# Kernel optimization log

Hardware: AMD Instinct MI355X
Metric: run time of the kernel (lower is better)

The kernel has to match this reference:

```python
import jax, jax.numpy as jnp
import numpy as np

N_NODES = 50000
N_EDGES = 150000
D = 512
N_LAYERS = 4
BN_EPS = 1e-5


def setup_inputs() -> dict:
    key = jax.random.key(0)
    ks = jax.random.split(key, 8)
    scale = 1.0 / np.sqrt(D)
    x = jax.random.normal(ks[0], (N_NODES, D), dtype=jnp.float32)
    W1 = jax.random.normal(ks[1], (N_LAYERS, D, D), dtype=jnp.float32) * scale
    b1 = jax.random.normal(ks[2], (N_LAYERS, D), dtype=jnp.float32) * 0.01
    gamma = jnp.ones((N_LAYERS, D), dtype=jnp.float32)
    beta = jnp.zeros((N_LAYERS, D), dtype=jnp.float32)
    W2 = jax.random.normal(ks[3], (N_LAYERS, D, D), dtype=jnp.float32) * scale
    b2 = jax.random.normal(ks[4], (N_LAYERS, D), dtype=jnp.float32) * 0.01
    src = jax.random.randint(ks[5], (N_EDGES,), 0, N_NODES, dtype=jnp.int32)
    dst = jax.random.randint(ks[6], (N_EDGES,), 0, N_NODES, dtype=jnp.int32)
    return {"x": x, "W1": W1, "b1": b1, "gamma": gamma, "beta": beta,
            "W2": W2, "b2": b2, "src": src, "dst": dst}


def _gin_layer(h, src, dst, W1, b1, gamma, beta, W2, b2):
    # GIN sum aggregation: agg[v] = sum_{(u->v) in E} h[u]; eps = 0
    agg = jax.ops.segment_sum(h[src], dst, num_segments=N_NODES)
    z = jnp.dot(h + agg, W1.T) + b1                      # [N, D] Linear1
    # BatchNorm1d (training mode: batch stats, biased variance)
    mu = jnp.mean(z, axis=0)
    var = jnp.mean(jnp.square(z - mu), axis=0)
    z = (z - mu) * jax.lax.rsqrt(var + BN_EPS) * gamma + beta
    z = jax.nn.relu(z)
    return jnp.dot(z, W2.T) + b2                          # [N, D] Linear2


def reference(x, W1, b1, gamma, beta, W2, b2, src, dst):
    h = x
    outs = []
    for i in range(N_LAYERS):
        h = _gin_layer(h, src, dst, W1[i], b1[i], gamma[i], beta[i], W2[i], b2[i])
        outs.append(h)
    # single graph: dgl.mean_nodes == mean over all nodes, squeeze -> [D]
    return (jnp.mean(outs[-1], axis=0), jnp.mean(outs[-2], axis=0))
```

## Files before the change

### kernel.cpp

```cpp
#include <hip/hip_runtime.h>

#define NN 50000
#define MPAD 50176
#define DD 512
#define NE 150000

typedef float f32x2 __attribute__((ext_vector_type(2)));
typedef float f32x4 __attribute__((ext_vector_type(4)));
typedef float f32x8 __attribute__((ext_vector_type(8)));
typedef __bf16 bf16x8 __attribute__((ext_vector_type(8)));
typedef unsigned short u16x8 __attribute__((ext_vector_type(8)));
typedef unsigned int u32x2 __attribute__((ext_vector_type(2)));

__device__ __forceinline__ void gload16(const void* g, void* l) {
  __builtin_amdgcn_global_load_lds((const __attribute__((address_space(1))) void*)g,
                                   (__attribute__((address_space(3))) void*)l, 16, 0, 0);
}

__device__ __forceinline__ u32x2 f32x8_to_fp8(f32x8 v) {
  int t0 = __builtin_amdgcn_cvt_pk_fp8_f32(v[0], v[1], 0, false);
  t0 = __builtin_amdgcn_cvt_pk_fp8_f32(v[2], v[3], t0, true);
  int t1 = __builtin_amdgcn_cvt_pk_fp8_f32(v[4], v[5], 0, false);
  t1 = __builtin_amdgcn_cvt_pk_fp8_f32(v[6], v[7], t1, true);
  u32x2 r;
  r[0] = (unsigned)t0;
  r[1] = (unsigned)t1;
  return r;
}
__device__ __forceinline__ f32x8 fp8x8_to_f32(u32x2 u) {
  f32x2 a = __builtin_amdgcn_cvt_pk_f32_fp8((int)u[0], false);
  f32x2 b = __builtin_amdgcn_cvt_pk_f32_fp8((int)u[0], true);
  f32x2 c = __builtin_amdgcn_cvt_pk_f32_fp8((int)u[1], false);
  f32x2 d = __builtin_amdgcn_cvt_pk_f32_fp8((int)u[1], true);
  f32x8 v;
  v[0]=a[0]; v[1]=a[1]; v[2]=b[0]; v[3]=b[1]; v[4]=c[0]; v[5]=c[1]; v[6]=d[0]; v[7]=d[1];
  return v;
}

#define READ_FRAGS(la, lb, kk, AV, BV)                                                       \
  {                                                                                          \
    const int so = (((kk) * 4 + fg) ^ sx) * 8;                                               \
    _Pragma("unroll") for (int i = 0; i < 4; ++i)                                            \
        AV[i] = *reinterpret_cast<const bf16x8*>(&(la)[(rg + i * 16 + fr) * 64 + so]);       \
    _Pragma("unroll") for (int j = 0; j < 4; ++j)                                            \
        BV[j] = *reinterpret_cast<const bf16x8*>(&(lb)[(cg + j * 16 + fr) * 64 + so]);       \
  }

#define MFMA16(AV, BV)                                                                       \
  _Pragma("unroll") for (int i = 0; i < 4; ++i)                                              \
      _Pragma("unroll") for (int j = 0; j < 4; ++j)                                          \
          acc[i][j] = __builtin_amdgcn_mfma_f32_16x16x32_bf16(AV[i], BV[j], acc[i][j], 0, 0, 0);

#define PHASE_TAIL(AV, BV)                                                                   \
  __builtin_amdgcn_s_barrier();                                                              \
  asm volatile("s_waitcnt lgkmcnt(0)" ::: "memory");                                         \
  __builtin_amdgcn_sched_barrier(0);                                                         \
  __builtin_amdgcn_s_setprio(1);                                                             \
  MFMA16(AV, BV);                                                                            \
  __builtin_amdgcn_s_setprio(0);

__global__ __launch_bounds__(256) void prep1_k(
    const float* __restrict__ x, const float* __restrict__ W1,
    const int* __restrict__ dst, unsigned char* __restrict__ xq,
    unsigned short* __restrict__ wb1, int* __restrict__ cnt,
    unsigned short* __restrict__ xact, float* __restrict__ stats,
    float* __restrict__ cs2, float* __restrict__ cs3) {
  const int b = blockIdx.x;
  const int tid = threadIdx.x;
  if (b < 12500) {
    const size_t i = ((size_t)b * 256 + tid) * 8;
    const f32x4* g = reinterpret_cast<const f32x4*>(x + i);
    f32x4 a = g[0], c = g[1];
    f32x8 v;
    v[0]=a[0]; v[1]=a[1]; v[2]=a[2]; v[3]=a[3]; v[4]=c[0]; v[5]=c[1]; v[6]=c[2]; v[7]=c[3];
    *reinterpret_cast<u32x2*>(xq + i) = f32x8_to_fp8(v);
  } else if (b < 12628) {
    const size_t i = ((size_t)(b - 12500) * 256 + tid) * 8;
    const f32x4* g = reinterpret_cast<const f32x4*>(W1 + i);
    f32x4 a = g[0], c = g[1];
    f32x8 v;
    v[0]=a[0]; v[1]=a[1]; v[2]=a[2]; v[3]=a[3]; v[4]=c[0]; v[5]=c[1]; v[6]=c[2]; v[7]=c[3];
    *reinterpret_cast<bf16x8*>(wb1 + i) = __builtin_convertvector(v, bf16x8);
  } else if (b < 13214) {
    const int e = (b - 12628) * 256 + tid;
    if (e < NE) atomicAdd(&cnt[dst[e]], 1);
  } else if (b < 13258) {
    const int i = (b - 13214) * 256 + tid;
    u16x8 zz = {};
    *reinterpret_cast<u16x8*>(xact + (size_t)NN * DD + (size_t)i * 8) = zz;
  } else {
    for (int i = tid; i < 2 * DD; i += 256) stats[i] = 0.f;
    for (int i = tid; i < DD; i += 256) {
      cs2[i] = 0.f;
      cs3[i] = 0.f;
    }
  }
}

__global__ __launch_bounds__(1024) void scan_k(const int* __restrict__ cnt,
                                               int* __restrict__ rowptr,
                                               int* __restrict__ cursor) {
  __shared__ int wsum[16];
  __shared__ int base_s;
  if (threadIdx.x == 0) base_s = 0;
  __syncthreads();
  const int lane = threadIdx.x & 63;
  const int wid = threadIdx.x >> 6;
  for (int c0 = 0; c0 < NN; c0 += 1024) {
    const int i = c0 + threadIdx.x;
    const int v = (i < NN) ? cnt[i] : 0;
    int incl = v;
#pragma unroll
    for (int d = 1; d < 64; d <<= 1) {
      int t = __shfl_up(incl, d);
      if (lane >= d) incl += t;
    }
    if (lane == 63) wsum[wid] = incl;
    __syncthreads();
    if (wid == 0 && lane < 16) {
      int wv = wsum[lane];
#pragma unroll
      for (int d = 1; d < 16; d <<= 1) {
        int t = __shfl_up(wv, d);
        if (lane >= d) wv += t;
      }
      wsum[lane] = wv;
    }
    __syncthreads();
    const int waveoff = wid ? wsum[wid - 1] : 0;
    const int excl = base_s + waveoff + incl - v;
    if (i < NN) {
      rowptr[i] = excl;
      cursor[i] = excl;
    }
    __syncthreads();
    if (threadIdx.x == 0) base_s += wsum[15];
    __syncthreads();
  }
  if (threadIdx.x == 0) rowptr[NN] = base_s;
}

__global__ __launch_bounds__(256) void prep2_k(
    const int* __restrict__ src, const int* __restrict__ dst,
    int* __restrict__ cursor, int* __restrict__ csrc,
    const float* __restrict__ W2, float* __restrict__ W2T) {
  __shared__ float t[64][65];
  const int b = blockIdx.x;
  const int tid = threadIdx.x;
  if (b < 586) {
    const int e = b * 256 + tid;
    if (e < NE) {
      const int pos = atomicAdd(&cursor[dst[e]], 1);
      csrc[pos] = src[e];
    }
  } else {
    const int q = b - 586;
    const int l = q >> 6;
    const int rem = q & 63;
    const int a0 = (rem >> 3) * 64;
    const int b0 = (rem & 7) * 64;
    const float* sp = W2 + (size_t)l * DD * DD;
    float* dp = W2T + (size_t)l * DD * DD;
#pragma unroll
    for (int k = 0; k < 16; ++k) {
      const int idx = k * 256 + tid;
      const int r = idx >> 6, c = idx & 63;
      t[r][c] = sp[(size_t)(a0 + r) * DD + b0 + c];
    }
    __syncthreads();
#pragma unroll
    for (int k = 0; k < 16; ++k) {
      const int idx = k * 256 + tid;
      const int r = idx >> 6, c = idx & 63;
      dp[(size_t)(b0 + r) * DD + a0 + c] = t[c][r];
    }
  }
}

__global__ __launch_bounds__(256) void prep3_k(
    const float* __restrict__ W1all, const float* __restrict__ W2T,
    unsigned short* __restrict__ WF, const float* __restrict__ b2all,
    float* __restrict__ cvec, const int* __restrict__ rowptr,
    float* __restrict__ degp1) {
  __shared__ char pl[36864];
  const int b = blockIdx.x;
  const int tid = threadIdx.x;
  if (b < 48) {
    constexpr int LDK = 72;
    unsigned short* lA = (unsigned short*)pl;
    unsigned short* lB = (unsigned short*)(pl + 18432);
    const int l = b >> 4;
    const int rem = b & 15;
    const int brow = (rem >> 2) * 128;
    const int bcol = (rem & 3) * 128;
    const float* A = W1all + (size_t)(l + 1) * DD * DD;
    const float* Bt = W2T + (size_t)l * DD * DD;
    unsigned short* out = WF + (size_t)l * DD * DD;
    const int lane = tid & 63;
    const int w = tid >> 6;
    const int wr = (w >> 1) * 64;
    const int wc = (w & 1) * 64;
    const int fr = lane & 15;
    const int fg = lane >> 4;
    f32x4 acc[4][4] = {};
    const int srow = tid >> 3;
    const int scol = (tid & 7) * 8;
    for (int kt = 0; kt < 8; ++kt) {
      const int k0 = kt * 64 + scol;
      __syncthreads();
#pragma unroll
      for (int p = 0; p < 4; ++p) {
        const int r = srow + 32 * p;
        {
          const f32x4* g = reinterpret_cast<const f32x4*>(A + (size_t)(brow + r) * DD + k0);
          f32x4 v0 = g[0], v1 = g[1];
          f32x8 vf;
          vf[0]=v0[0]; vf[1]=v0[1]; vf[2]=v0[2]; vf[3]=v0[3];
          vf[4]=v1[0]; vf[5]=v1[1]; vf[6]=v1[2]; vf[7]=v1[3];
          *reinterpret_cast<bf16x8*>(&lA[r * LDK + scol]) = __builtin_convertvector(vf, bf16x8);
        }
        {
          const f32x4* g = reinterpret_cast<const f32x4*>(Bt + (size_t)(bcol + r) * DD + k0);
          f32x4 v0 = g[0], v1 = g[1];
          f32x8 vf;
          vf[0]=v0[0]; vf[1]=v0[1]; vf[2]=v0[2]; vf[3]=v0[3];
          vf[4]=v1[0]; vf[5]=v1[1]; vf[6]=v1[2]; vf[7]=v1[3];
          *reinterpret_cast<bf16x8*>(&lB[r * LDK + scol]) = __builtin_convertvector(vf, bf16x8);
        }
      }
      __syncthreads();
#pragma unroll
      for (int kk = 0; kk < 2; ++kk) {
        bf16x8 av[4], bv[4];
#pragma unroll
        for (int i = 0; i < 4; ++i)
          av[i] = *reinterpret_cast<const bf16x8*>(&lA[(wr + i * 16 + fr) * LDK + kk * 32 + fg * 8]);
#pragma unroll
        for (int j = 0; j < 4; ++j)
          bv[j] = *reinterpret_cast<const bf16x8*>(&lB[(wc + j * 16 + fr) * LDK + kk * 32 + fg * 8]);
#pragma unroll
        for (int i = 0; i < 4; ++i)
#pragma unroll
          for (int j = 0; j < 4; ++j)
            acc[i][j] = __builtin_amdgcn_mfma_f32_16x16x32_bf16(av[i], bv[j], acc[i][j], 0, 0, 0);
      }
    }
#pragma unroll
    for (int j = 0; j < 4; ++j) {
      const int col = bcol + wc + j * 16 + fr;
#pragma unroll
      for (int i = 0; i < 4; ++i) {
        const int rb = brow + wr + i * 16 + fg * 4;
#pragma unroll
        for (int r = 0; r < 4; ++r) {
          __bf16 bb = (__bf16)acc[i][j][r];
          out[(size_t)(rb + r) * DD + col] = __builtin_bit_cast(unsigned short, bb);
        }
      }
    }
  } else if (b < 51) {
    const int l = b - 48;
    float* bb = (float*)pl;
    bb[tid] = b2all[(size_t)l * DD + tid];
    bb[tid + 256] = b2all[(size_t)l * DD + tid + 256];
    __syncthreads();
#pragma unroll
    for (int rep = 0; rep < 2; ++rep) {
      const int n = tid + rep * 256;
      const float* row = W1all + (size_t)(l + 1) * DD * DD + (size_t)n * DD;
      float s = 0.f;
      for (int a = 0; a < DD; a += 4) {
        f32x4 v = *reinterpret_cast<const f32x4*>(row + a);
        s += v[0] * bb[a] + v[1] * bb[a + 1] + v[2] * bb[a + 2] + v[3] * bb[a + 3];
      }
      cvec[l * DD + n] = s;
    }
  } else {
    const int i = (b - 51) * 256 + tid;
    if (i < MPAD) degp1[i] = (i < NN) ? (float)(1 + rowptr[i + 1] - rowptr[i]) : 0.f;
  }
}

__global__ __launch_bounds__(256) void agg_x_k(const unsigned char* __restrict__ xq,
                                               const int* __restrict__ rowptr,
                                               const int* __restrict__ csrc,
                                               unsigned short* __restrict__ xout) {
  const int node = blockIdx.x * 4 + (threadIdx.x >> 6);
  const int lane = threadIdx.x & 63;
  const int c0 = lane * 8;
  f32x8 acc = fp8x8_to_f32(*reinterpret_cast<const u32x2*>(xq + (size_t)node * DD + c0));
  f32x8 acc2 = {};
  const int p1 = rowptr[node + 1];
  int p = rowptr[node];
  for (; p + 1 < p1; p += 2) {
    const int s0 = csrc[p];
    const int s1 = csrc[p + 1];
    u32x2 r0 = *reinterpret_cast<const u32x2*>(xq + (size_t)s0 * DD + c0);
    u32x2 r1 = *reinterpret_cast<const u32x2*>(xq + (size_t)s1 * DD + c0);
    acc += fp8x8_to_f32(r0);
    acc2 += fp8x8_to_f32(r1);
  }
  if (p < p1) {
    const int s0 = csrc[p];
    acc += fp8x8_to_f32(*reinterpret_cast<const u32x2*>(xq + (size_t)s0 * DD + c0));
  }
  acc += acc2;
  *reinterpret_cast<bf16x8*>(xout + (size_t)node * DD + c0) =
      __builtin_convertvector(acc, bf16x8);
}

__global__ __launch_bounds__(256) void agg_act_k(const unsigned char* __restrict__ z,
                                                 const float* __restrict__ scsh,
                                                 const int* __restrict__ rowptr,
                                                 const int* __restrict__ csrc,
                                                 unsigned short* __restrict__ xout) {
  const int node = blockIdx.x * 4 + (threadIdx.x >> 6);
  const int lane = threadIdx.x & 63;
  const int c0 = lane * 8;
  f32x4 sca = *reinterpret_cast<const f32x4*>(scsh + c0);
  f32x4 scb = *reinterpret_cast<const f32x4*>(scsh + c0 + 4);
  f32x4 sha = *reinterpret_cast<const f32x4*>(scsh + DD + c0);
  f32x4 shb = *reinterpret_cast<const f32x4*>(scsh + DD + c0 + 4);
#define ACT8(dst, uv)                                                    \
  {                                                                      \
    f32x8 f_ = fp8x8_to_f32(uv);                                         \
    _Pragma("unroll") for (int q = 0; q < 4; ++q) {                      \
      dst[q]     += fmaxf(f_[q]     * sca[q] + sha[q], 0.f);             \
      dst[q + 4] += fmaxf(f_[q + 4] * scb[q] + shb[q], 0.f);             \
    }                                                                    \
  }
  f32x8 acc = {}, acc2 = {};
  u32x2 sv = *reinterpret_cast<const u32x2*>(z + (size_t)node * DD + c0);
  ACT8(acc, sv)
  const int p1 = rowptr[node + 1];
  int p = rowptr[node];
  for (; p + 1 < p1; p += 2) {
    const int s0 = csrc[p];
    const int s1 = csrc[p + 1];
    u32x2 r0 = *reinterpret_cast<const u32x2*>(z + (size_t)s0 * DD + c0);
    u32x2 r1 = *reinterpret_cast<const u32x2*>(z + (size_t)s1 * DD + c0);
    ACT8(acc, r0)
    ACT8(acc2, r1)
  }
  if (p < p1) {
    const int s0 = csrc[p];
    u32x2 r0 = *reinterpret_cast<const u32x2*>(z + (size_t)s0 * DD + c0);
    ACT8(acc, r0)
  }
  acc += acc2;
#undef ACT8
  *reinterpret_cast<bf16x8*>(xout + (size_t)node * DD + c0) =
      __builtin_convertvector(acc, bf16x8);
}

__global__ __launch_bounds__(256) void colsum_act_k(const unsigned char* __restrict__ z,
                                                    const float* __restrict__ scsh,
                                                    float* __restrict__ cs) {
  __shared__ float red[4][DD];
  const int g = threadIdx.x >> 6;
  const int lane = threadIdx.x & 63;
  const int c0 = lane * 8;
  f32x4 sca = *reinterpret_cast<const f32x4*>(scsh + c0);
  f32x4 scb = *reinterpret_cast<const f32x4*>(scsh + c0 + 4);
  f32x4 sha = *reinterpret_cast<const f32x4*>(scsh + DD + c0);
  f32x4 shb = *reinterpret_cast<const f32x4*>(scsh + DD + c0 + 4);
  f32x8 acc = {};
  for (int rr = g; rr < 128; rr += 4) {
    const int row = blockIdx.x * 128 + rr;
    if (row < NN) {
      u32x2 rv = *reinterpret_cast<const u32x2*>(z + (size_t)row * DD + c0);
      f32x8 f = fp8x8_to_f32(rv);
#pragma unroll
      for (int q = 0; q < 4; ++q) {
        acc[q]     += fmaxf(f[q]     * sca[q] + sha[q], 0.f);
        acc[q + 4] += fmaxf(f[q + 4] * scb[q] + shb[q], 0.f);
      }
    }
  }
#pragma unroll
  for (int q = 0; q < 8; ++q) red[g][c0 + q] = acc[q];
  __syncthreads();
  for (int cc = threadIdx.x; cc < DD; cc += 256) {
    const float s = red[0][cc] + red[1][cc] + red[2][cc] + red[3][cc];
    atomicAdd(&cs[cc], s);
  }
}

__global__ void bnfin_k(float* __restrict__ stats, const float* __restrict__ gamma,
                        const float* __restrict__ beta, float* __restrict__ scsh) {
  const int n = threadIdx.x;
  const float inv = 1.0f / (float)NN;
  const float mu = stats[n] * inv;
  const float var = stats[DD + n] * inv - mu * mu;
  const float sc = rsqrtf(var + 1e-5f) * gamma[n];
  scsh[n] = sc;
  scsh[DD + n] = beta[n] - mu * sc;
  stats[n] = 0.f;
  stats[DD + n] = 0.f;
}

__global__ __launch_bounds__(512, 2) void gemmf_k(
    const unsigned short* __restrict__ A, const unsigned short* __restrict__ B,
    unsigned char* __restrict__ Z, float* __restrict__ stats,
    const float* __restrict__ degp1, const float* __restrict__ cvec) {
  __shared__ unsigned short sm[73728];
  constexpr int AOFF[3] = {0, 16384, 8192};
  constexpr int BOFF[3] = {24576, 57344, 40960};
  const int tid = threadIdx.x;
  const int lane = tid & 63;
  const int w = tid >> 6;
  const int rg = (w >> 2) * 64;
  const int cg = (w & 3) * 64;
  const int fr = lane & 15;
  const int fg = lane >> 4;
  const int sx = fr & 7;
  const int bid = blockIdx.x;
  const int swb = (bid & 7) * 98 + (bid >> 3);
  const int brow = (swb >> 1) * 128;
  const int bcol = (swb & 1) * 256;
  const char* Ab = (const char*)A + (size_t)brow * 1024;
  const char* Bb = (const char*)B + (size_t)bcol * 1024;
  const int srow = tid >> 3;
  const int sce = (tid & 7) * 8;
  const int sswz = (((tid & 7) ^ (srow & 7))) * 16;

  f32x4 acc[4][4] = {};

#pragma unroll
  for (int t = 0; t < 2; ++t) {
#pragma unroll
    for (int i = 0; i < 2; ++i)
      gload16(Ab + (size_t)(i * 64 + srow) * 1024 + t * 128 + sswz,
              &sm[AOFF[t] + (i * 64 + srow) * 64 + sce]);
#pragma unroll
    for (int i = 0; i < 4; ++i)
      gload16(Bb + (size_t)(i * 64 + srow) * 1024 + t * 128 + sswz,
              &sm[BOFF[t] + (i * 64 + srow) * 64 + sce]);
  }

#pragma unroll
  for (int kt = 0; kt < 8; ++kt) {
    if (kt < 7) asm volatile("s_waitcnt vmcnt(6)" ::: "memory");
    else        asm volatile("s_waitcnt vmcnt(0)" ::: "memory");
    __builtin_amdgcn_s_barrier();
    const unsigned short* la = &sm[AOFF[kt % 3]];
    const unsigned short* lb = &sm[BOFF[kt % 3]];
    bf16x8 av[4], bv[4];
    READ_FRAGS(la, lb, 0, av, bv);
    if (kt + 2 < 8) {
      const int t2 = kt + 2;
#pragma unroll
      for (int i = 0; i < 2; ++i)
        gload16(Ab + (size_t)(i * 64 + srow) * 1024 + t2 * 128 + sswz,
                &sm[AOFF[t2 % 3] + (i * 64 + srow) * 64 + sce]);
      gload16(Bb + (size_t)srow * 1024 + t2 * 128 + sswz,
              &sm[BOFF[t2 % 3] + srow * 64 + sce]);
    }
    PHASE_TAIL(av, bv)
    __builtin_amdgcn_s_barrier();
    READ_FRAGS(la, lb, 1, av, bv);
    if (kt + 2 < 8) {
      const int t2 = kt + 2;
#pragma unroll
      for (int i = 1; i < 4; ++i)
        gload16(Bb + (size_t)(i * 64 + srow) * 1024 + t2 * 128 + sswz,
                &sm[BOFF[t2 % 3] + (i * 64 + srow) * 64 + sce]);
    }
    PHASE_TAIL(av, bv)
  }

  if (cvec != nullptr) {
    float cj[4];
#pragma unroll
    for (int j = 0; j < 4; ++j) cj[j] = cvec[bcol + cg + j * 16 + fr];
#pragma unroll
    for (int i = 0; i < 4; ++i)
#pragma unroll
      for (int r = 0; r < 4; ++r) {
        const float dgv = degp1[brow + rg + i * 16 + fg * 4 + r];
#pragma unroll
        for (int j = 0; j < 4; ++j) acc[i][j][r] += dgv * cj[j];
      }
  }

#pragma unroll
  for (int j = 0; j < 4; ++j) {
    const int col = bcol + cg + j * 16 + fr;
    float s1 = 0.f, s2 = 0.f;
#pragma unroll
    for (int i = 0; i < 4; ++i)
#pragma unroll
      for (int r = 0; r < 4; ++r) {
        const float v = acc[i][j][r];
        s1 += v;
        s2 += v * v;
      }
    s1 += __shfl_down(s1, 32);
    s2 += __shfl_down(s2, 32);
    s1 += __shfl_down(s1, 16);
    s2 += __shfl_down(s2, 16);
    if (lane < 16) {
      atomicAdd(&stats[col], s1);
      atomicAdd(&stats[DD + col], s2);
    }
  }

  unsigned short* C = &sm[24576];
#pragma unroll
  for (int j = 0; j < 4; ++j)
#pragma unroll
    for (int i = 0; i < 4; ++i)
#pragma unroll
      for (int r = 0; r < 4; ++r) {
        const int row = rg + i * 16 + fg * 4 + r;
        const int col = cg + j * 16 + fr;
        __bf16 b = (__bf16)acc[i][j][r];
        C[row * 256 + (((col >> 3) ^ (row & 7)) << 3) + (col & 7)] =
            __builtin_bit_cast(unsigned short, b);
      }
  asm volatile("s_waitcnt lgkmcnt(0)" ::: "memory");
  __builtin_amdgcn_s_barrier();
  const int orow = tid >> 2;
  const int ox = orow & 7;
  const unsigned short* cr = &C[orow * 256];
  unsigned char* zg = Z + (size_t)(brow + orow) * DD + bcol;
#pragma unroll
  for (int i = 0; i < 8; ++i) {
    const int s = (tid & 3) * 8 + ((i + tid) & 7);
    u16x8 cv = *reinterpret_cast<const u16x8*>(cr + (s ^ ox) * 8);
    f32x8 cf = __builtin_convertvector(__builtin_bit_cast(bf16x8, cv), f32x8);
    *reinterpret_cast<u32x2*>(zg + s * 8) = f32x8_to_fp8(cf);
  }
}

__global__ __launch_bounds__(256) void out_k(const float* __restrict__ cs3,
                                             const float* __restrict__ cs2,
                                             const float* __restrict__ W2all,
                                             const float* __restrict__ b2all,
                                             float* __restrict__ out) {
  const int o = blockIdx.x * 4 + (threadIdx.x >> 6);
  const int lane = threadIdx.x & 63;
  const int layer = (o < DD) ? 3 : 2;
  const int n = o & (DD - 1);
  const float* cs = (o < DD) ? cs3 : cs2;
  const float* row = W2all + (size_t)layer * DD * DD + (size_t)n * DD + lane * 8;
  f32x4 w0 = *reinterpret_cast<const f32x4*>(row);
  f32x4 w1 = *reinterpret_cast<const f32x4*>(row + 4);
  f32x4 c0 = *reinterpret_cast<const f32x4*>(cs + lane * 8);
  f32x4 c1 = *reinterpret_cast<const f32x4*>(cs + lane * 8 + 4);
  float s = w0[0]*c0[0] + w0[1]*c0[1] + w0[2]*c0[2] + w0[3]*c0[3]
          + w1[0]*c1[0] + w1[1]*c1[1] + w1[2]*c1[2] + w1[3]*c1[3];
#pragma unroll
  for (int d = 32; d > 0; d >>= 1) s += __shfl_down(s, d);
  if (lane == 0) out[o] = s / (float)NN + b2all[layer * DD + n];
}

extern "C" void kernel_launch(void* const* d_in, const int* in_sizes, int n_in,
                              void* d_out, int out_size, void* d_ws, size_t ws_size,
                              hipStream_t stream) {
  const float* x     = (const float*)d_in[0];
  const float* W1    = (const float*)d_in[1];
  const float* gamma = (const float*)d_in[3];
  const float* beta  = (const float*)d_in[4];
  const float* W2    = (const float*)d_in[5];
  const float* b2    = (const float*)d_in[6];
  const int*   src   = (const int*)d_in[7];
  const int*   dst   = (const int*)d_in[8];
  float* out = (float*)d_out;

  char* ws = (char*)d_ws;
  unsigned short* xact   = (unsigned short*)(ws);
  unsigned char*  z      = (unsigned char*)(ws + 51380224);
  unsigned char*  xq     = (unsigned char*)(ws + 77070336);
  unsigned short* wb1    = (unsigned short*)(ws + 102670336);
  unsigned short* wf     = (unsigned short*)(ws + 103194624);
  float*          w2t    = (float*)(ws + 104767488);
  float*          cvec   = (float*)(ws + 107913216);
  float*          cs2    = (float*)(ws + 107921408);
  float*          cs3    = (float*)(ws + 107923456);
  float*          stats  = (float*)(ws + 107925504);
  float*          scsh   = (float*)(ws + 107929600);
  float*          degp1  = (float*)(ws + 107933696);
  int*            rowptr = (int*)(ws + 108134400);
  int*            cursor = (int*)(ws + 108334592);
  int*            csrc   = (int*)(ws + 108534784);

  hipMemsetAsync(cursor, 0, NN * sizeof(int), stream);
  prep1_k<<<13259, 256, 0, stream>>>(x, W1, dst, xq, wb1, cursor, xact, stats, cs2, cs3);
  scan_k<<<1, 1024, 0, stream>>>(cursor, rowptr, cursor);
  prep2_k<<<778, 256, 0, stream>>>(src, dst, cursor, csrc, W2, w2t);
  prep3_k<<<247, 256, 0, stream>>>(W1, w2t, wf, b2, cvec, rowptr, degp1);

  agg_x_k<<<NN / 4, 256, 0, stream>>>(xq, rowptr, csrc, xact);
  gemmf_k<<<784, 512, 0, stream>>>(xact, wb1, z, stats, degp1, nullptr);
  bnfin_k<<<1, DD, 0, stream>>>(stats, gamma, beta, scsh);

  for (int l = 0; l < 3; ++l) {
    agg_act_k<<<NN / 4, 256, 0, stream>>>(z, scsh, rowptr, csrc, xact);
    if (l == 2) colsum_act_k<<<392, 256, 0, stream>>>(z, scsh, cs2);
    gemmf_k<<<784, 512, 0, stream>>>(xact, wf + (size_t)l * DD * DD, z, stats,
                                     degp1, cvec + l * DD);
    bnfin_k<<<1, DD, 0, stream>>>(stats, gamma + (l + 1) * DD, beta + (l + 1) * DD, scsh);
  }

  colsum_act_k<<<392, 256, 0, stream>>>(z, scsh, cs3);
  out_k<<<256, 256, 0, stream>>>(cs3, cs2, W2, b2, out);
}
```

Baseline: 530.6 us.

## Fold BN finalize into consumers, per-layer stats, smaller GEMM tiles

Removes the single-block bnfin_k launches by keeping a separate stats buffer per layer and having agg_act_k and colsum_act_k compute the BN scale and shift inline from the raw sums. The layer-2 column sum is folded into agg_act_k through an LDS reduction and atomics, which drops one colsum pass over z. The GEMM is retiled from 128x256 to 128x128 with a double-buffered two-stage pipeline, less LDS and occupancy 4, doubling the grid to 1568 blocks. The tradeoffs are more per-block scale and shift recomputation, the extra atomics, and a simpler pipeline with full vmcnt(0) waits that may overlap loads less well.

New measurement: 726.7 us. 37.0% more time.

```diff
diff --git a/kernel.cpp b/kernel.cpp
--- a/kernel.cpp
+++ b/kernel.cpp
@@ -37,33 +37,37 @@
   return v;
 }
 
-#define READ_FRAGS(la, lb, kk, AV, BV)                                                       \
-  {                                                                                          \
-    const int so = (((kk) * 4 + fg) ^ sx) * 8;                                               \
-    _Pragma("unroll") for (int i = 0; i < 4; ++i)                                            \
-        AV[i] = *reinterpret_cast<const bf16x8*>(&(la)[(rg + i * 16 + fr) * 64 + so]);       \
-    _Pragma("unroll") for (int j = 0; j < 4; ++j)                                            \
-        BV[j] = *reinterpret_cast<const bf16x8*>(&(lb)[(cg + j * 16 + fr) * 64 + so]);       \
-  }
-
-#define MFMA16(AV, BV)                                                                       \
-  _Pragma("unroll") for (int i = 0; i < 4; ++i)                                              \
-      _Pragma("unroll") for (int j = 0; j < 4; ++j)                                          \
-          acc[i][j] = __builtin_amdgcn_mfma_f32_16x16x32_bf16(AV[i], BV[j], acc[i][j], 0, 0, 0);
-
-#define PHASE_TAIL(AV, BV)                                                                   \
-  __builtin_amdgcn_s_barrier();                                                              \
-  asm volatile("s_waitcnt lgkmcnt(0)" ::: "memory");                                         \
-  __builtin_amdgcn_sched_barrier(0);                                                         \
-  __builtin_amdgcn_s_setprio(1);                                                             \
-  MFMA16(AV, BV);                                                                            \
-  __builtin_amdgcn_s_setprio(0);
+__device__ __forceinline__ void mk_scsh(const float* __restrict__ stL,
+                                        const float* __restrict__ gm,
+                                        const float* __restrict__ bt, int c0,
+                                        f32x4& sca, f32x4& scb, f32x4& sha, f32x4& shb) {
+  const float inv = 1.0f / (float)NN;
+  f32x4 s1a = *reinterpret_cast<const f32x4*>(stL + c0);
+  f32x4 s1b = *reinterpret_cast<const f32x4*>(stL + c0 + 4);
+  f32x4 s2a = *reinterpret_cast<const f32x4*>(stL + DD + c0);
+  f32x4 s2b = *reinterpret_cast<const f32x4*>(stL + DD + c0 + 4);
+  f32x4 ga = *reinterpret_cast<const f32x4*>(gm + c0);
+  f32x4 gb = *reinterpret_cast<const f32x4*>(gm + c0 + 4);
+  f32x4 ba = *reinterpret_cast<const f32x4*>(bt + c0);
+  f32x4 bb = *reinterpret_cast<const f32x4*>(bt + c0 + 4);
+#pragma unroll
+  for (int q = 0; q < 4; ++q) {
+    float mu = s1a[q] * inv;
+    float var = s2a[q] * inv - mu * mu;
+    sca[q] = rsqrtf(var + 1e-5f) * ga[q];
+    sha[q] = ba[q] - mu * sca[q];
+    mu = s1b[q] * inv;
+    var = s2b[q] * inv - mu * mu;
+    scb[q] = rsqrtf(var + 1e-5f) * gb[q];
+    shb[q] = bb[q] - mu * scb[q];
+  }
+}
 
 __global__ __launch_bounds__(256) void prep1_k(
     const float* __restrict__ x, const float* __restrict__ W1,
     const int* __restrict__ dst, unsigned char* __restrict__ xq,
     unsigned short* __restrict__ wb1, int* __restrict__ cnt,
-    unsigned short* __restrict__ xact, float* __restrict__ stats,
+    unsigned short* __restrict__ xact, float* __restrict__ statsL,
     float* __restrict__ cs2, float* __restrict__ cs3) {
   const int b = blockIdx.x;
   const int tid = threadIdx.x;
@@ -89,7 +93,7 @@
     u16x8 zz = {};
     *reinterpret_cast<u16x8*>(xact + (size_t)NN * DD + (size_t)i * 8) = zz;
   } else {
-    for (int i = tid; i < 2 * DD; i += 256) stats[i] = 0.f;
+    for (int i = tid; i < 8 * DD; i += 256) statsL[i] = 0.f;
     for (int i = tid; i < DD; i += 256) {
       cs2[i] = 0.f;
       cs3[i] = 0.f;
@@ -310,17 +314,20 @@
 }
 
 __global__ __launch_bounds__(256) void agg_act_k(const unsigned char* __restrict__ z,
-                                                 const float* __restrict__ scsh,
+                                                 const float* __restrict__ stL,
+                                                 const float* __restrict__ gm,
+                                                 const float* __restrict__ bt,
                                                  const int* __restrict__ rowptr,
                                                  const int* __restrict__ csrc,
-                                                 unsigned short* __restrict__ xout) {
+                                                 unsigned short* __restrict__ xout,
+                                                 float* __restrict__ cs) {
+  __shared__ float red[4][DD];
   const int node = blockIdx.x * 4 + (threadIdx.x >> 6);
+  const int wid = threadIdx.x >> 6;
   const int lane = threadIdx.x & 63;
   const int c0 = lane * 8;
-  f32x4 sca = *reinterpret_cast<const f32x4*>(scsh + c0);
-  f32x4 scb = *reinterpret_cast<const f32x4*>(scsh + c0 + 4);
-  f32x4 sha = *reinterpret_cast<const f32x4*>(scsh + DD + c0);
-  f32x4 shb = *reinterpret_cast<const f32x4*>(scsh + DD + c0 + 4);
+  f32x4 sca, scb, sha, shb;
+  mk_scsh(stL, gm, bt, c0, sca, scb, sha, shb);
 #define ACT8(dst, uv)                                                    \
   {                                                                      \
     f32x8 f_ = fp8x8_to_f32(uv);                                         \
@@ -332,6 +339,15 @@
   f32x8 acc = {}, acc2 = {};
   u32x2 sv = *reinterpret_cast<const u32x2*>(z + (size_t)node * DD + c0);
   ACT8(acc, sv)
+  if (cs != nullptr) {
+#pragma unroll
+    for (int q = 0; q < 8; ++q) red[wid][c0 + q] = acc[q];
+    __syncthreads();
+    for (int cc = threadIdx.x; cc < DD; cc += 256) {
+      const float s = red[0][cc] + red[1][cc] + red[2][cc] + red[3][cc];
+      atomicAdd(&cs[cc], s);
+    }
+  }
   const int p1 = rowptr[node + 1];
   int p = rowptr[node];
   for (; p + 1 < p1; p += 2) {
@@ -354,16 +370,16 @@
 }
 
 __global__ __launch_bounds__(256) void colsum_act_k(const unsigned char* __restrict__ z,
-                                                    const float* __restrict__ scsh,
+                                                    const float* __restrict__ stL,
+                                                    const float* __restrict__ gm,
+                                                    const float* __restrict__ bt,
                                                     float* __restrict__ cs) {
   __shared__ float red[4][DD];
   const int g = threadIdx.x >> 6;
   const int lane = threadIdx.x & 63;
   const int c0 = lane * 8;
-  f32x4 sca = *reinterpret_cast<const f32x4*>(scsh + c0);
-  f32x4 scb = *reinterpret_cast<const f32x4*>(scsh + c0 + 4);
-  f32x4 sha = *reinterpret_cast<const f32x4*>(scsh + DD + c0);
-  f32x4 shb = *reinterpret_cast<const f32x4*>(scsh + DD + c0 + 4);
+  f32x4 sca, scb, sha, shb;
+  mk_scsh(stL, gm, bt, c0, sca, scb, sha, shb);
   f32x8 acc = {};
   for (int rr = g; rr < 128; rr += 4) {
     const int row = blockIdx.x * 128 + rr;
@@ -386,105 +402,89 @@
   }
 }
 
-__global__ void bnfin_k(float* __restrict__ stats, const float* __restrict__ gamma,
-                        const float* __restrict__ beta, float* __restrict__ scsh) {
-  const int n = threadIdx.x;
-  const float inv = 1.0f / (float)NN;
-  const float mu = stats[n] * inv;
-  const float var = stats[DD + n] * inv - mu * mu;
-  const float sc = rsqrtf(var + 1e-5f) * gamma[n];
-  scsh[n] = sc;
-  scsh[DD + n] = beta[n] - mu * sc;
-  stats[n] = 0.f;
-  stats[DD + n] = 0.f;
-}
-
-__global__ __launch_bounds__(512, 2) void gemmf_k(
+__global__ __launch_bounds__(512, 4) void gemmf_k(
     const unsigned short* __restrict__ A, const unsigned short* __restrict__ B,
     unsigned char* __restrict__ Z, float* __restrict__ stats,
     const float* __restrict__ degp1, const float* __restrict__ cvec) {
-  __shared__ unsigned short sm[73728];
-  constexpr int AOFF[3] = {0, 16384, 8192};
-  constexpr int BOFF[3] = {24576, 57344, 40960};
+  __shared__ unsigned short sm[32768];
   const int tid = threadIdx.x;
   const int lane = tid & 63;
   const int w = tid >> 6;
   const int rg = (w >> 2) * 64;
-  const int cg = (w & 3) * 64;
+  const int cg = (w & 3) * 32;
   const int fr = lane & 15;
   const int fg = lane >> 4;
   const int sx = fr & 7;
   const int bid = blockIdx.x;
-  const int swb = (bid & 7) * 98 + (bid >> 3);
-  const int brow = (swb >> 1) * 128;
-  const int bcol = (swb & 1) * 256;
+  const int swb = (bid & 7) * 196 + (bid >> 3);
+  const int brow = (swb >> 2) * 128;
+  const int bcol = (swb & 3) * 128;
   const char* Ab = (const char*)A + (size_t)brow * 1024;
   const char* Bb = (const char*)B + (size_t)bcol * 1024;
   const int srow = tid >> 3;
   const int sce = (tid & 7) * 8;
   const int sswz = (((tid & 7) ^ (srow & 7))) * 16;
 
-  f32x4 acc[4][4] = {};
-
-#pragma unroll
-  for (int t = 0; t < 2; ++t) {
-#pragma unroll
-    for (int i = 0; i < 2; ++i)
-      gload16(Ab + (size_t)(i * 64 + srow) * 1024 + t * 128 + sswz,
-              &sm[AOFF[t] + (i * 64 + srow) * 64 + sce]);
-#pragma unroll
-    for (int i = 0; i < 4; ++i)
-      gload16(Bb + (size_t)(i * 64 + srow) * 1024 + t * 128 + sswz,
-              &sm[BOFF[t] + (i * 64 + srow) * 64 + sce]);
-  }
+  f32x4 acc[4][2] = {};
+
+#define STG(t, b)                                                                    \
+  _Pragma("unroll") for (int i = 0; i < 2; ++i) {                                    \
+    gload16(Ab + (size_t)(i * 64 + srow) * 1024 + (t) * 128 + sswz,                  \
+            &sm[(b) * 8192 + (i * 64 + srow) * 64 + sce]);                           \
+    gload16(Bb + (size_t)(i * 64 + srow) * 1024 + (t) * 128 + sswz,                  \
+            &sm[16384 + (b) * 8192 + (i * 64 + srow) * 64 + sce]);                   \
+  }
+
+  STG(0, 0)
 
 #pragma unroll
   for (int kt = 0; kt < 8; ++kt) {
-    if (kt < 7) asm volatile("s_waitcnt vmcnt(6)" ::: "memory");
-    else        asm volatile("s_waitcnt vmcnt(0)" ::: "memory");
+    asm volatile("s_waitcnt vmcnt(0)" ::: "memory");
     __builtin_amdgcn_s_barrier();
-    const unsigned short* la = &sm[AOFF[kt % 3]];
-    const unsigned short* lb = &sm[BOFF[kt % 3]];
-    bf16x8 av[4], bv[4];
-    READ_FRAGS(la, lb, 0, av, bv);
-    if (kt + 2 < 8) {
-      const int t2 = kt + 2;
-#pragma unroll
-      for (int i = 0; i < 2; ++i)
-        gload16(Ab + (size_t)(i * 64 + srow) * 1024 + t2 * 128 + sswz,
-                &sm[AOFF[t2 % 3] + (i * 64 + srow) * 64 + sce]);
-      gload16(Bb + (size_t)srow * 1024 + t2 * 128 + sswz,
-              &sm[BOFF[t2 % 3] + srow * 64 + sce]);
-    }
-    PHASE_TAIL(av, bv)
-    __builtin_amdgcn_s_barrier();
-    READ_FRAGS(la, lb, 1, av, bv);
-    if (kt + 2 < 8) {
-      const int t2 = kt + 2;
-#pragma unroll
-      for (int i = 1; i < 4; ++i)
-        gload16(Bb + (size_t)(i * 64 + srow) * 1024 + t2 * 128 + sswz,
-                &sm[BOFF[t2 % 3] + (i * 64 + srow) * 64 + sce]);
-    }
-    PHASE_TAIL(av, bv)
-  }
+    if (kt < 7) STG(kt + 1, (kt + 1) & 1)
+    const unsigned short* la = &sm[(kt & 1) * 8192];
+    const unsigned short* lb = &sm[16384 + (kt & 1) * 8192];
+    bf16x8 av[2][4], bv[2][2];
+#pragma unroll
+    for (int kk = 0; kk < 2; ++kk) {
+      const int so = ((kk * 4 + fg) ^ sx) * 8;
+#pragma unroll
+      for (int i = 0; i < 4; ++i)
+        av[kk][i] = *reinterpret_cast<const bf16x8*>(&la[(rg + i * 16 + fr) * 64 + so]);
+#pragma unroll
+      for (int j = 0; j < 2; ++j)
+        bv[kk][j] = *reinterpret_cast<const bf16x8*>(&lb[(cg + j * 16 + fr) * 64 + so]);
+    }
+    asm volatile("s_waitcnt lgkmcnt(0)" ::: "memory");
+    __builtin_amdgcn_sched_barrier(0);
+    __builtin_amdgcn_s_setprio(1);
+#pragma unroll
+    for (int kk = 0; kk < 2; ++kk)
+#pragma unroll
+      for (int i = 0; i < 4; ++i)
+#pragma unroll
+        for (int j = 0; j < 2; ++j)
+          acc[i][j] = __builtin_amdgcn_mfma_f32_16x16x32_bf16(av[kk][i], bv[kk][j], acc[i][j], 0, 0, 0);
+    __builtin_amdgcn_s_setprio(0);
+  }
+#undef STG
 
   if (cvec != nullptr) {
-    float cj[4];
-#pragma unroll
-    for (int j = 0; j < 4; ++j) cj[j] = cvec[bcol + cg + j * 16 + fr];
+    float cj[2];
+#pragma unroll
+    for (int j = 0; j < 2; ++j) cj[j] = cvec[bcol + cg + j * 16 + fr];
 #pragma unroll
     for (int i = 0; i < 4; ++i)
 #pragma unroll
       for (int r = 0; r < 4; ++r) {
         const float dgv = degp1[brow + rg + i * 16 + fg * 4 + r];
 #pragma unroll
-        for (int j = 0; j < 4; ++j) acc[i][j][r] += dgv * cj[j];
-      }
-  }
-
-#pragma unroll
-  for (int j = 0; j < 4; ++j) {
+        for (int j = 0; j < 2; ++j) acc[i][j][r] += dgv * cj[j];
+      }
+  }
+
+#pragma unroll
+  for (int j = 0; j < 2; ++j) {
     const int col = bcol + cg + j * 16 + fr;
     float s1 = 0.f, s2 = 0.f;
 #pragma unroll
@@ -505,9 +505,10 @@
     }
   }
 
-  unsigned short* C = &sm[24576];
-#pragma unroll
-  for (int j = 0; j < 4; ++j)
+  __builtin_amdgcn_s_barrier();
+  unsigned short* C = sm;
+#pragma unroll
+  for (int j = 0; j < 2; ++j)
 #pragma unroll
     for (int i = 0; i < 4; ++i)
 #pragma unroll
@@ -515,18 +516,18 @@
         const int row = rg + i * 16 + fg * 4 + r;
         const int col = cg + j * 16 + fr;
         __bf16 b = (__bf16)acc[i][j][r];
-        C[row * 256 + (((col >> 3) ^ (row & 7)) << 3) + (col & 7)] =
+        C[row * 128 + (((col >> 3) ^ (row & 7)) << 3) + (col & 7)] =
             __builtin_bit_cast(unsigned short, b);
       }
   asm volatile("s_waitcnt lgkmcnt(0)" ::: "memory");
   __builtin_amdgcn_s_barrier();
   const int orow = tid >> 2;
   const int ox = orow & 7;
-  const unsigned short* cr = &C[orow * 256];
+  const unsigned short* cr = &C[orow * 128];
   unsigned char* zg = Z + (size_t)(brow + orow) * DD + bcol;
 #pragma unroll
-  for (int i = 0; i < 8; ++i) {
-    const int s = (tid & 3) * 8 + ((i + tid) & 7);
+  for (int i = 0; i < 4; ++i) {
+    const int s = (tid & 3) * 4 + ((i + tid) & 3);
     u16x8 cv = *reinterpret_cast<const u16x8*>(cr + (s ^ ox) * 8);
     f32x8 cf = __builtin_convertvector(__builtin_bit_cast(bf16x8, cv), f32x8);
     *reinterpret_cast<u32x2*>(zg + s * 8) = f32x8_to_fp8(cf);
@@ -578,31 +579,32 @@
   float*          cvec   = (float*)(ws + 107913216);
   float*          cs2    = (float*)(ws + 107921408);
   float*          cs3    = (float*)(ws + 107923456);
-  float*          stats  = (float*)(ws + 107925504);
-  float*          scsh   = (float*)(ws + 107929600);
-  float*          degp1  = (float*)(ws + 107933696);
-  int*            rowptr = (int*)(ws + 108134400);
-  int*            cursor = (int*)(ws + 108334592);
-  int*            csrc   = (int*)(ws + 108534784);
+  float*          statsL = (float*)(ws + 107925504);
+  float*          degp1  = (float*)(ws + 107941888);
+  int*            rowptr = (int*)(ws + 108142592);
+  int*            cursor = (int*)(ws + 108342784);
+  int*            csrc   = (int*)(ws + 108542976);
 
   hipMemsetAsync(cursor, 0, NN * sizeof(int), stream);
-  prep1_k<<<13259, 256, 0, stream>>>(x, W1, dst, xq, wb1, cursor, xact, stats, cs2, cs3);
+  prep1_k<<<13259, 256, 0, stream>>>(x, W1, dst, xq, wb1, cursor, xact, statsL, cs2, cs3);
   scan_k<<<1, 1024, 0, stream>>>(cursor, rowptr, cursor);
   prep2_k<<<778, 256, 0, stream>>>(src, dst, cursor, csrc, W2, w2t);
   prep3_k<<<247, 256, 0, stream>>>(W1, w2t, wf, b2, cvec, rowptr, degp1);
 
   agg_x_k<<<NN / 4, 256, 0, stream>>>(xq, rowptr, csrc, xact);
-  gemmf_k<<<784, 512, 0, stream>>>(xact, wb1, z, stats, degp1, nullptr);
-  bnfin_k<<<1, DD, 0, stream>>>(stats, gamma, beta, scsh);
+  gemmf_k<<<1568, 512, 0, stream>>>(xact, wb1, z, statsL, degp1, nullptr);
 
   for (int l = 0; l < 3; ++l) {
-    agg_act_k<<<NN / 4, 256, 0, stream>>>(z, scsh, rowptr, csrc, xact);
-    if (l == 2) colsum_act_k<<<392, 256, 0, stream>>>(z, scsh, cs2);
-    gemmf_k<<<784, 512, 0, stream>>>(xact, wf + (size_t)l * DD * DD, z, stats,
-                                     degp1, cvec + l * DD);
-    bnfin_k<<<1, DD, 0, stream>>>(stats, gamma + (l + 1) * DD, beta + (l + 1) * DD, scsh);
-  }
-
-  colsum_act_k<<<392, 256, 0, stream>>>(z, scsh, cs3);
+    agg_act_k<<<NN / 4, 256, 0, stream>>>(z, statsL + (size_t)l * 2 * DD,
+                                          gamma + (size_t)l * DD, beta + (size_t)l * DD,
+                                          rowptr, csrc, xact,
+                                          (l == 2) ? cs2 : nullptr);
+    gemmf_k<<<1568, 512, 0, stream>>>(xact, wf + (size_t)l * DD * DD, z,
+                                      statsL + (size_t)(l + 1) * 2 * DD, degp1,
+                                      cvec + l * DD);
+  }
+
+  colsum_act_k<<<392, 256, 0, stream>>>(z, statsL + 3 * 2 * DD,
+                                        gamma + 3 * DD, beta + 3 * DD, cs3);
   out_k<<<256, 256, 0, stream>>>(cs3, cs2, W2, b2, out);
 }
```
